# Optimization experiments

Hardware: AMD Instinct MI355X
Metric: run time of the kernel (lower is better)

The kernel has to match this reference:

```python
import jax, jax.numpy as jnp
import numpy as np

M = 2  # sqrt(n_heads)

def setup_inputs() -> dict:
    key = jax.random.key(0)
    k1, k2, k3 = jax.random.split(key, 3)
    b, H, W, c = 8, 256, 256, 64
    x = jax.random.normal(k1, (b, H, W, c), dtype=jnp.float32)
    # 1x1 conv weights expressed as matrices: qkv [c, 3c], project [c, c]
    scale = 1.0 / np.sqrt(c)
    Wqkv = jax.random.normal(k2, (c, 3 * c), dtype=jnp.float32) * scale
    Wproj = jax.random.normal(k3, (c, c), dtype=jnp.float32) * scale
    return {"x": x, "Wqkv": Wqkv, "Wproj": Wproj}


def reference(x, Wqkv, Wproj):
    b, H, W, c = x.shape
    h, w = H // M, W // M
    temp = c ** (-0.5)  # n_features ** -0.5
    # 1x1 conv qkv projection (bias-free)
    qkv = jnp.einsum('byxc,cd->byxd', x, Wqkv)  # [b,H,W,3c]
    q, k, v = jnp.split(qkv, 3, axis=-1)

    def blk(t):
        # 'b (h m1) (w m2) c -> b (m1 m2) c (h w)'
        t = t.reshape(b, h, M, w, M, c)
        t = t.transpose(0, 2, 4, 5, 1, 3)  # b m1 m2 c h w
        return t.reshape(b, M * M, c, h * w)

    q, k, v = blk(q), blk(k), blk(v)
    # channel-attention: c x c score per block, contracted over hw
    score = jnp.einsum('bncl,bndl->bncd', q, k) * temp
    weight = jax.nn.softmax(score, axis=-1)
    out = jnp.einsum('bncd,bndl->bncl', weight, v)
    # inverse rearrange: 'b (m1 m2) c (h w) -> b (h m1) (w m2) c'
    out = out.reshape(b, M, M, c, h, w).transpose(0, 4, 1, 5, 2, 3).reshape(b, H, W, c)
    # 1x1 conv output projection
    return jnp.einsum('byxc,cd->byxd', out, Wproj)
```

## Files before the change

kernel.cpp:

```cpp
#include <hip/hip_runtime.h>

typedef float f32x4 __attribute__((ext_vector_type(4)));
typedef __bf16 bf16x8 __attribute__((ext_vector_type(8)));
typedef short s16x8 __attribute__((ext_vector_type(8)));

__device__ __forceinline__ unsigned short f2bf(float f) {
  unsigned u = __builtin_bit_cast(unsigned, f);
  return (unsigned short)((u + 0x7fffu + ((u >> 16) & 1u)) >> 16);
}
__device__ __forceinline__ float bf2f(unsigned short s) {
  unsigned u = ((unsigned)s) << 16;
  return __builtin_bit_cast(float, u);
}

#define LSTR 40

__global__ __launch_bounds__(256) void gram_kernel(const float* __restrict__ x,
                                                   float* __restrict__ G) {
  __shared__ unsigned short xsh[64 * LSTR];
  __shared__ unsigned short xsl[64 * LSTR];
  const int tid = threadIdx.x;
  const int lane = tid & 63;
  const int wave = tid >> 6;
  const int blk = blockIdx.x;
  const int chunk = blk & 31;
  const int bn = blk >> 5;
  const int b = bn >> 2;
  const int m1 = (bn >> 1) & 1;
  const int m2 = bn & 1;
  const int px0 = (tid & 15) * 2;
  const int c0 = (tid >> 4) * 4;
  const int mrow = lane & 15;
  const int k8 = (lane >> 4) * 8;
  const int tr0 = (wave >> 1) * 2;
  const int tc0 = (wave & 1) * 2;

  f32x4 acc[2][2];
#pragma unroll
  for (int i = 0; i < 2; ++i)
#pragma unroll
    for (int j = 0; j < 2; ++j) acc[i][j] = (f32x4){0.f, 0.f, 0.f, 0.f};

  for (int ks = 0; ks < 16; ++ks) {
    int l0 = chunk * 512 + ks * 32 + px0;
    int hy = l0 >> 7, wx = l0 & 127;
    int y = 2 * hy + m1, xx = 2 * wx + m2;
    const float* p0 = x + ((b * 256 + y) * 256 + xx) * 64 + c0;
    f32x4 v0 = *(const f32x4*)p0;
    f32x4 v1 = *(const f32x4*)(p0 + 128);
    __syncthreads();
#pragma unroll
    for (int i = 0; i < 4; ++i) {
      unsigned short h0 = f2bf(v0[i]), h1 = f2bf(v1[i]);
      unsigned short g0 = f2bf(v0[i] - bf2f(h0)), g1 = f2bf(v1[i] - bf2f(h1));
      *(unsigned*)&xsh[(c0 + i) * LSTR + px0] = (unsigned)h0 | ((unsigned)h1 << 16);
      *(unsigned*)&xsl[(c0 + i) * LSTR + px0] = (unsigned)g0 | ((unsigned)g1 << 16);
    }
    __syncthreads();
    s16x8 rh[2], rl[2], qh[2], ql[2];
#pragma unroll
    for (int i = 0; i < 2; ++i) {
      rh[i] = *(const s16x8*)&xsh[(16 * (tr0 + i) + mrow) * LSTR + k8];
      rl[i] = *(const s16x8*)&xsl[(16 * (tr0 + i) + mrow) * LSTR + k8];
      qh[i] = *(const s16x8*)&xsh[(16 * (tc0 + i) + mrow) * LSTR + k8];
      ql[i] = *(const s16x8*)&xsl[(16 * (tc0 + i) + mrow) * LSTR + k8];
    }
#pragma unroll
    for (int i = 0; i < 2; ++i)
#pragma unroll
      for (int j = 0; j < 2; ++j) {
        bf16x8 ah = __builtin_bit_cast(bf16x8, rh[i]);
        bf16x8 al = __builtin_bit_cast(bf16x8, rl[i]);
        bf16x8 bh = __builtin_bit_cast(bf16x8, qh[j]);
        bf16x8 bl = __builtin_bit_cast(bf16x8, ql[j]);
        acc[i][j] = __builtin_amdgcn_mfma_f32_16x16x32_bf16(ah, bh, acc[i][j], 0, 0, 0);
        acc[i][j] = __builtin_amdgcn_mfma_f32_16x16x32_bf16(ah, bl, acc[i][j], 0, 0, 0);
        acc[i][j] = __builtin_amdgcn_mfma_f32_16x16x32_bf16(al, bh, acc[i][j], 0, 0, 0);
      }
  }
  float* Gp = G + bn * 4096;
#pragma unroll
  for (int i = 0; i < 2; ++i)
#pragma unroll
    for (int j = 0; j < 2; ++j)
#pragma unroll
      for (int r = 0; r < 4; ++r) {
        int row = 16 * (tr0 + i) + (lane >> 4) * 4 + r;
        int col = 16 * (tc0 + j) + (lane & 15);
        atomicAdd(&Gp[row * 64 + col], acc[i][j][r]);
      }
}

__device__ __forceinline__ void mm64(const float* Ab, int ars, int acs,
                                     const float* Bb, float* Dst, int ds,
                                     float scale, int ti4, int tj4) {
  float acc[4][4] = {};
  for (int kk = 0; kk < 64; ++kk) {
    float av[4];
#pragma unroll
    for (int i = 0; i < 4; ++i) av[i] = Ab[(ti4 + i) * ars + kk * acs];
#pragma unroll
    for (int j = 0; j < 4; ++j) {
      float bv = Bb[kk * 68 + tj4 + j];
#pragma unroll
      for (int i = 0; i < 4; ++i) acc[i][j] += av[i] * bv;
    }
  }
#pragma unroll
  for (int i = 0; i < 4; ++i)
#pragma unroll
    for (int j = 0; j < 4; ++j) Dst[(ti4 + i) * ds + tj4 + j] = scale * acc[i][j];
}

__global__ __launch_bounds__(256) void fuse_kernel(const float* __restrict__ G,
                                                   const float* __restrict__ Wqkv,
                                                   const float* __restrict__ Wproj,
                                                   float* __restrict__ F) {
  __shared__ float A[64 * 68];
  __shared__ float B[64 * 68];
  __shared__ float T[64 * 68];
  const int tid = threadIdx.x;
  const int bn = blockIdx.x;
  const int ti4 = (tid >> 4) * 4, tj4 = (tid & 15) * 4;

  for (int i = tid; i < 4096; i += 256) {
    int r = i >> 6, c = i & 63;
    A[r * 68 + c] = G[bn * 4096 + i];
    B[r * 68 + c] = Wqkv[r * 192 + 64 + c];
  }
  __syncthreads();
  mm64(A, 68, 1, B, T, 68, 1.f, ti4, tj4);
  __syncthreads();
  for (int i = tid; i < 4096; i += 256) {
    int r = i >> 6, c = i & 63;
    B[r * 68 + c] = Wqkv[r * 192 + c];
  }
  __syncthreads();
  mm64(B, 1, 68, T, A, 68, 0.125f, ti4, tj4);
  __syncthreads();
  if (tid < 64) {
    float mx = -1e30f;
    for (int d = 0; d < 64; ++d) mx = fmaxf(mx, A[tid * 68 + d]);
    float s = 0.f;
    for (int d = 0; d < 64; ++d) {
      float e = __expf(A[tid * 68 + d] - mx);
      A[tid * 68 + d] = e;
      s += e;
    }
    float inv = 1.f / s;
    for (int d = 0; d < 64; ++d) A[tid * 68 + d] *= inv;
  }
  __syncthreads();
  for (int i = tid; i < 4096; i += 256) {
    int r = i >> 6, c = i & 63;
    B[r * 68 + c] = Wproj[i];
  }
  __syncthreads();
  mm64(A, 1, 68, B, T, 68, 1.f, ti4, tj4);
  __syncthreads();
  for (int i = tid; i < 4096; i += 256) {
    int r = i >> 6, c = i & 63;
    B[r * 68 + c] = Wqkv[r * 192 + 128 + c];
  }
  __syncthreads();
  mm64(B, 68, 1, T, F + bn * 4096, 64, 1.f, ti4, tj4);
}

__global__ __launch_bounds__(256) void out_kernel(const float* __restrict__ x,
                                                  const float* __restrict__ F,
                                                  float* __restrict__ out) {
  const int tid = threadIdx.x;
  const int lane = tid & 63;
  const int wave = tid >> 6;
  const int blk = blockIdx.x;
  const int hyg = blk & 63;
  const int bn = blk >> 6;
  const int b = bn >> 2;
  const int m1 = (bn >> 1) & 1;
  const int m2 = bn & 1;

  s16x8 bh[2][4], bl[2][4];
  const float* Fp = F + bn * 4096;
#pragma unroll
  for (int ksj = 0; ksj < 2; ++ksj)
#pragma unroll
    for (int tc = 0; tc < 4; ++tc) {
      s16x8 hv, lv;
#pragma unroll
      for (int j = 0; j < 8; ++j) {
        int k = ksj * 32 + (lane >> 4) * 8 + j;
        int e = tc * 16 + (lane & 15);
        float f = Fp[k * 64 + e];
        unsigned short hb = f2bf(f);
        hv[j] = (short)hb;
        lv[j] = (short)f2bf(f - bf2f(hb));
      }
      bh[ksj][tc] = hv;
      bl[ksj][tc] = lv;
    }

  for (int r = 0; r < 2; ++r) {
    int hy = hyg * 2 + r;
    int y = 2 * hy + m1;
    const float* xrow = x + ((b * 256 + y) * 256) * 64;
    float* orow = out + ((b * 256 + y) * 256) * 64;
#pragma unroll
    for (int ptI = 0; ptI < 2; ++ptI) {
      int pt = wave + ptI * 4;
      int wx = pt * 16 + (lane & 15);
      int xx = 2 * wx + m2;
      const float* pp = xrow + xx * 64 + (lane >> 4) * 8;
      s16x8 ah[2], al[2];
#pragma unroll
      for (int ksj = 0; ksj < 2; ++ksj) {
        f32x4 u0 = *(const f32x4*)(pp + ksj * 32);
        f32x4 u1 = *(const f32x4*)(pp + ksj * 32 + 4);
        s16x8 hv, lv;
#pragma unroll
        for (int j = 0; j < 4; ++j) {
          unsigned short hb0 = f2bf(u0[j]);
          unsigned short hb1 = f2bf(u1[j]);
          hv[j] = (short)hb0;
          hv[4 + j] = (short)hb1;
          lv[j] = (short)f2bf(u0[j] - bf2f(hb0));
          lv[4 + j] = (short)f2bf(u1[j] - bf2f(hb1));
        }
        ah[ksj] = hv;
        al[ksj] = lv;
      }
      f32x4 acc[4];
#pragma unroll
      for (int tc = 0; tc < 4; ++tc) acc[tc] = (f32x4){0.f, 0.f, 0.f, 0.f};
#pragma unroll
      for (int ksj = 0; ksj < 2; ++ksj)
#pragma unroll
        for (int tc = 0; tc < 4; ++tc) {
          bf16x8 A_h = __builtin_bit_cast(bf16x8, ah[ksj]);
          bf16x8 A_l = __builtin_bit_cast(bf16x8, al[ksj]);
          bf16x8 B_h = __builtin_bit_cast(bf16x8, bh[ksj][tc]);
          bf16x8 B_l = __builtin_bit_cast(bf16x8, bl[ksj][tc]);
          acc[tc] = __builtin_amdgcn_mfma_f32_16x16x32_bf16(A_h, B_h, acc[tc], 0, 0, 0);
          acc[tc] = __builtin_amdgcn_mfma_f32_16x16x32_bf16(A_h, B_l, acc[tc], 0, 0, 0);
          acc[tc] = __builtin_amdgcn_mfma_f32_16x16x32_bf16(A_l, B_h, acc[tc], 0, 0, 0);
        }
#pragma unroll
      for (int tc = 0; tc < 4; ++tc)
#pragma unroll
        for (int j = 0; j < 4; ++j) {
          int prow = (lane >> 4) * 4 + j;
          int xx2 = 2 * (pt * 16 + prow) + m2;
          orow[xx2 * 64 + tc * 16 + (lane & 15)] = acc[tc][j];
        }
    }
  }
}

extern "C" void kernel_launch(void* const* d_in, const int* in_sizes, int n_in,
                              void* d_out, int out_size, void* d_ws, size_t ws_size,
                              hipStream_t stream) {
  (void)in_sizes; (void)n_in; (void)out_size; (void)ws_size;
  const float* x = (const float*)d_in[0];
  const float* Wqkv = (const float*)d_in[1];
  const float* Wproj = (const float*)d_in[2];
  float* out = (float*)d_out;
  float* G = (float*)d_ws;
  float* F = G + 32 * 4096;

  hipMemsetAsync(G, 0, 32 * 4096 * sizeof(float), stream);
  gram_kernel<<<1024, 256, 0, stream>>>(x, G);
  fuse_kernel<<<32, 256, 0, stream>>>(G, Wqkv, Wproj, F);
  out_kernel<<<2048, 256, 0, stream>>>(x, F, out);
}
```

Before: 286.0 us.

## Prefetch full image rows in gram kernel and pre-split F into bf16 hi/lo

The gram kernel now stages one full 128-pixel row per round instead of 32-pixel slices. Each thread loads 64 contiguous bytes per pixel, and the next row's global loads are issued before the current row's MFMA work so that memory latency overlaps compute. This cuts the number of barriers from 16 pairs to 4 and uses a larger LDS tile. Separately, the fuse kernel now emits F already transposed and split into bf16 high and low halves, so the out kernel does vector loads instead of strided scalar loads plus per-block conversion. The risks are higher register pressure from holding 8 float4 prefetches, and possible LDS bank conflicts with the new stride.

```diff
diff --git a/kernel.cpp b/kernel.cpp
--- a/kernel.cpp
+++ b/kernel.cpp
@@ -13,12 +13,12 @@
   return __builtin_bit_cast(float, u);
 }
 
-#define LSTR 40
+#define PSTR 136
 
 __global__ __launch_bounds__(256) void gram_kernel(const float* __restrict__ x,
                                                    float* __restrict__ G) {
-  __shared__ unsigned short xsh[64 * LSTR];
-  __shared__ unsigned short xsl[64 * LSTR];
+  __shared__ unsigned short xsh[64 * PSTR];
+  __shared__ unsigned short xsl[64 * PSTR];
   const int tid = threadIdx.x;
   const int lane = tid & 63;
   const int wave = tid >> 6;
@@ -28,8 +28,9 @@
   const int b = bn >> 2;
   const int m1 = (bn >> 1) & 1;
   const int m2 = bn & 1;
-  const int px0 = (tid & 15) * 2;
-  const int c0 = (tid >> 4) * 4;
+  const int p0 = (tid & 63) * 2;
+  const int c0 = (tid >> 6) * 16;
+  const int xx = 2 * p0 + m2;
   const int mrow = lane & 15;
   const int k8 = (lane >> 4) * 8;
   const int tr0 = (wave >> 1) * 2;
@@ -41,42 +42,62 @@
 #pragma unroll
     for (int j = 0; j < 2; ++j) acc[i][j] = (f32x4){0.f, 0.f, 0.f, 0.f};
 
-  for (int ks = 0; ks < 16; ++ks) {
-    int l0 = chunk * 512 + ks * 32 + px0;
-    int hy = l0 >> 7, wx = l0 & 127;
-    int y = 2 * hy + m1, xx = 2 * wx + m2;
-    const float* p0 = x + ((b * 256 + y) * 256 + xx) * 64 + c0;
-    f32x4 v0 = *(const f32x4*)p0;
-    f32x4 v1 = *(const f32x4*)(p0 + 128);
+  f32x4 v[8];
+  {
+    int y = 2 * (chunk * 4) + m1;
+    const float* p = x + ((b * 256 + y) * 256 + xx) * 64 + c0;
+#pragma unroll
+    for (int i = 0; i < 4; ++i) {
+      v[i] = ((const f32x4*)p)[i];
+      v[4 + i] = ((const f32x4*)(p + 128))[i];
+    }
+  }
+
+#pragma unroll
+  for (int round = 0; round < 4; ++round) {
     __syncthreads();
 #pragma unroll
-    for (int i = 0; i < 4; ++i) {
-      unsigned short h0 = f2bf(v0[i]), h1 = f2bf(v1[i]);
-      unsigned short g0 = f2bf(v0[i] - bf2f(h0)), g1 = f2bf(v1[i] - bf2f(h1));
-      *(unsigned*)&xsh[(c0 + i) * LSTR + px0] = (unsigned)h0 | ((unsigned)h1 << 16);
-      *(unsigned*)&xsl[(c0 + i) * LSTR + px0] = (unsigned)g0 | ((unsigned)g1 << 16);
+    for (int i = 0; i < 16; ++i) {
+      float f0 = v[i >> 2][i & 3];
+      float f1 = v[4 + (i >> 2)][i & 3];
+      unsigned short h0 = f2bf(f0), h1 = f2bf(f1);
+      unsigned short g0 = f2bf(f0 - bf2f(h0)), g1 = f2bf(f1 - bf2f(h1));
+      *(unsigned*)&xsh[(c0 + i) * PSTR + p0] = (unsigned)h0 | ((unsigned)h1 << 16);
+      *(unsigned*)&xsl[(c0 + i) * PSTR + p0] = (unsigned)g0 | ((unsigned)g1 << 16);
     }
     __syncthreads();
-    s16x8 rh[2], rl[2], qh[2], ql[2];
-#pragma unroll
-    for (int i = 0; i < 2; ++i) {
-      rh[i] = *(const s16x8*)&xsh[(16 * (tr0 + i) + mrow) * LSTR + k8];
-      rl[i] = *(const s16x8*)&xsl[(16 * (tr0 + i) + mrow) * LSTR + k8];
-      qh[i] = *(const s16x8*)&xsh[(16 * (tc0 + i) + mrow) * LSTR + k8];
-      ql[i] = *(const s16x8*)&xsl[(16 * (tc0 + i) + mrow) * LSTR + k8];
-    }
-#pragma unroll
-    for (int i = 0; i < 2; ++i)
-#pragma unroll
-      for (int j = 0; j < 2; ++j) {
-        bf16x8 ah = __builtin_bit_cast(bf16x8, rh[i]);
-        bf16x8 al = __builtin_bit_cast(bf16x8, rl[i]);
-        bf16x8 bh = __builtin_bit_cast(bf16x8, qh[j]);
-        bf16x8 bl = __builtin_bit_cast(bf16x8, ql[j]);
-        acc[i][j] = __builtin_amdgcn_mfma_f32_16x16x32_bf16(ah, bh, acc[i][j], 0, 0, 0);
-        acc[i][j] = __builtin_amdgcn_mfma_f32_16x16x32_bf16(ah, bl, acc[i][j], 0, 0, 0);
-        acc[i][j] = __builtin_amdgcn_mfma_f32_16x16x32_bf16(al, bh, acc[i][j], 0, 0, 0);
-      }
+    if (round < 3) {
+      int y = 2 * (chunk * 4 + round + 1) + m1;
+      const float* p = x + ((b * 256 + y) * 256 + xx) * 64 + c0;
+#pragma unroll
+      for (int i = 0; i < 4; ++i) {
+        v[i] = ((const f32x4*)p)[i];
+        v[4 + i] = ((const f32x4*)(p + 128))[i];
+      }
+    }
+#pragma unroll
+    for (int kst = 0; kst < 4; ++kst) {
+      s16x8 rh[2], rl[2], qh[2], ql[2];
+#pragma unroll
+      for (int i = 0; i < 2; ++i) {
+        rh[i] = *(const s16x8*)&xsh[(16 * (tr0 + i) + mrow) * PSTR + kst * 32 + k8];
+        rl[i] = *(const s16x8*)&xsl[(16 * (tr0 + i) + mrow) * PSTR + kst * 32 + k8];
+        qh[i] = *(const s16x8*)&xsh[(16 * (tc0 + i) + mrow) * PSTR + kst * 32 + k8];
+        ql[i] = *(const s16x8*)&xsl[(16 * (tc0 + i) + mrow) * PSTR + kst * 32 + k8];
+      }
+#pragma unroll
+      for (int i = 0; i < 2; ++i)
+#pragma unroll
+        for (int j = 0; j < 2; ++j) {
+          bf16x8 ah = __builtin_bit_cast(bf16x8, rh[i]);
+          bf16x8 al = __builtin_bit_cast(bf16x8, rl[i]);
+          bf16x8 bh = __builtin_bit_cast(bf16x8, qh[j]);
+          bf16x8 bl = __builtin_bit_cast(bf16x8, ql[j]);
+          acc[i][j] = __builtin_amdgcn_mfma_f32_16x16x32_bf16(ah, bh, acc[i][j], 0, 0, 0);
+          acc[i][j] = __builtin_amdgcn_mfma_f32_16x16x32_bf16(ah, bl, acc[i][j], 0, 0, 0);
+          acc[i][j] = __builtin_amdgcn_mfma_f32_16x16x32_bf16(al, bh, acc[i][j], 0, 0, 0);
+        }
+    }
   }
   float* Gp = G + bn * 4096;
 #pragma unroll
@@ -115,7 +136,8 @@
 __global__ __launch_bounds__(256) void fuse_kernel(const float* __restrict__ G,
                                                    const float* __restrict__ Wqkv,
                                                    const float* __restrict__ Wproj,
-                                                   float* __restrict__ F) {
+                                                   unsigned short* __restrict__ Fh,
+                                                   unsigned short* __restrict__ Fl) {
   __shared__ float A[64 * 68];
   __shared__ float B[64 * 68];
   __shared__ float T[64 * 68];
@@ -163,11 +185,20 @@
     B[r * 68 + c] = Wqkv[r * 192 + 128 + c];
   }
   __syncthreads();
-  mm64(B, 68, 1, T, F + bn * 4096, 64, 1.f, ti4, tj4);
+  mm64(B, 68, 1, T, A, 68, 1.f, ti4, tj4);
+  __syncthreads();
+  for (int i = tid; i < 4096; i += 256) {
+    int f = i & 63, e = i >> 6;
+    float val = A[f * 68 + e];
+    unsigned short h = f2bf(val);
+    Fh[bn * 4096 + e * 64 + f] = h;
+    Fl[bn * 4096 + e * 64 + f] = f2bf(val - bf2f(h));
+  }
 }
 
 __global__ __launch_bounds__(256) void out_kernel(const float* __restrict__ x,
-                                                  const float* __restrict__ F,
+                                                  const unsigned short* __restrict__ Fh,
+                                                  const unsigned short* __restrict__ Fl,
                                                   float* __restrict__ out) {
   const int tid = threadIdx.x;
   const int lane = tid & 63;
@@ -180,24 +211,20 @@
   const int m2 = bn & 1;
 
   s16x8 bh[2][4], bl[2][4];
-  const float* Fp = F + bn * 4096;
-#pragma unroll
-  for (int ksj = 0; ksj < 2; ++ksj)
-#pragma unroll
-    for (int tc = 0; tc < 4; ++tc) {
-      s16x8 hv, lv;
-#pragma unroll
-      for (int j = 0; j < 8; ++j) {
-        int k = ksj * 32 + (lane >> 4) * 8 + j;
-        int e = tc * 16 + (lane & 15);
-        float f = Fp[k * 64 + e];
-        unsigned short hb = f2bf(f);
-        hv[j] = (short)hb;
-        lv[j] = (short)f2bf(f - bf2f(hb));
-      }
-      bh[ksj][tc] = hv;
-      bl[ksj][tc] = lv;
-    }
+  {
+    const unsigned short* Fhp = Fh + bn * 4096;
+    const unsigned short* Flp = Fl + bn * 4096;
+    const int e = lane & 15;
+    const int k0 = (lane >> 4) * 8;
+#pragma unroll
+    for (int ksj = 0; ksj < 2; ++ksj)
+#pragma unroll
+      for (int tc = 0; tc < 4; ++tc) {
+        int off = (tc * 16 + e) * 64 + ksj * 32 + k0;
+        bh[ksj][tc] = *(const s16x8*)&Fhp[off];
+        bl[ksj][tc] = *(const s16x8*)&Flp[off];
+      }
+  }
 
   for (int r = 0; r < 2; ++r) {
     int hy = hyg * 2 + r;
@@ -264,10 +291,11 @@
   const float* Wproj = (const float*)d_in[2];
   float* out = (float*)d_out;
   float* G = (float*)d_ws;
-  float* F = G + 32 * 4096;
+  unsigned short* Fh = (unsigned short*)(G + 32 * 4096);
+  unsigned short* Fl = Fh + 32 * 4096;
 
   hipMemsetAsync(G, 0, 32 * 4096 * sizeof(float), stream);
   gram_kernel<<<1024, 256, 0, stream>>>(x, G);
-  fuse_kernel<<<32, 256, 0, stream>>>(G, Wqkv, Wproj, F);
-  out_kernel<<<2048, 256, 0, stream>>>(x, F, out);
-}
+  fuse_kernel<<<32, 256, 0, stream>>>(G, Wqkv, Wproj, Fh, Fl);
+  out_kernel<<<2048, 256, 0, stream>>>(x, Fh, Fl, out);
+}
```

Measured after the change: 294.3 us. 2.9% more time.
